# Optimization experiments

Measured on AMD Instinct MI355X. Metric: run time of the kernel, lower is better.

## Reference

```python
import jax, jax.numpy as jnp
import numpy as np

B, H, N, M = 8192, 512, 1024, 128
EPS_COS = 1e-8   # torch cosine_similarity default eps
EPS_NORM = 1e-16 # normalization eps in forward


def _linear_params(key, fan_in, fan_out):
    # torch nn.Linear default init: U(-1/sqrt(fan_in), 1/sqrt(fan_in))
    lim = 1.0 / np.sqrt(fan_in)
    kw, kb = jax.random.split(key)
    W = jax.random.uniform(kw, (fan_out, fan_in), minval=-lim, maxval=lim, dtype=jnp.float32)
    b = jax.random.uniform(kb, (fan_out,), minval=-lim, maxval=lim, dtype=jnp.float32)
    return W, b


def setup_inputs() -> dict:
    key = jax.random.key(0)
    ks = jax.random.split(key, 8)
    Wk, bk = _linear_params(ks[0], H, M)
    Wb, bb = _linear_params(ks[1], H, 1)
    Wg, bg = _linear_params(ks[2], H, 1)
    Ws, bs = _linear_params(ks[3], H, N)
    Wgam, bgam = _linear_params(ks[4], H, 1)
    x = jax.random.normal(ks[5], (B, H), dtype=jnp.float32)
    # previous_state is an attention-weight vector over memory rows (sums to 1)
    previous_state = jax.nn.softmax(jax.random.normal(ks[6], (B, N), dtype=jnp.float32), axis=-1)
    memory = jax.random.normal(ks[7], (N, M), dtype=jnp.float32)
    return dict(x=x, previous_state=previous_state, memory=memory,
                Wk=Wk, bk=bk, Wb=Wb, bb=bb, Wg=Wg, bg=bg,
                Ws=Ws, bs=bs, Wgam=Wgam, bgam=bgam)


def _circular_convolution(w, s):
    # Full circular convolution over the memory axis:
    #   out[b, i] = sum_j w[b, j] * s[b, (i - j) mod N]
    # Implemented via FFT to avoid materializing a [B, N, N] shift matrix.
    out = jnp.fft.irfft(jnp.fft.rfft(w, axis=-1) * jnp.fft.rfft(s, axis=-1),
                        n=w.shape[-1], axis=-1)
    # conv of nonnegative weights is nonnegative; clamp tiny FFT round-off
    # negatives so the fractional power below stays well defined.
    return jnp.maximum(out, 0.0)


def reference(x, previous_state, memory, Wk, bk, Wb, bb, Wg, bg, Ws, bs, Wgam, bgam):
    k = x @ Wk.T + bk                                   # [B, M]
    beta = jax.nn.softplus(x @ Wb.T + bb)               # [B, 1]
    g = jax.nn.sigmoid(x @ Wg.T + bg)                   # [B, 1]
    s = jax.nn.softmax(x @ Ws.T + bs, axis=-1)          # [B, N]
    gamma = 1.0 + jax.nn.softplus(x @ Wgam.T + bgam)    # [B, 1]

    # cosine similarity between each key and each memory row -> [B, N]
    k_n = k / jnp.maximum(jnp.linalg.norm(k, axis=-1, keepdims=True), EPS_COS)
    m_n = memory / jnp.maximum(jnp.linalg.norm(memory, axis=-1, keepdims=True), EPS_COS)
    cos = k_n @ m_n.T                                   # [B, N]

    w_c = jax.nn.softmax(beta * cos, axis=1)            # content addressing
    w_g = g * w_c + (1.0 - g) * previous_state          # interpolation gate
    w_t = _circular_convolution(w_g, s)                 # location shift
    w = w_t ** gamma                                    # sharpening
    w = w / (jnp.sum(w, axis=1, keepdims=True) + EPS_NORM)

    read = w @ memory                                   # [B, M]
    return read, w
```

## Files before the change

### kernel.cpp

```cpp
#include <hip/hip_runtime.h>
#include <hip/hip_bf16.h>
#include <hip/hip_fp16.h>

typedef __attribute__((ext_vector_type(8))) short short8;
typedef __attribute__((ext_vector_type(4))) short short4v;
typedef __attribute__((ext_vector_type(4))) float f32x4;

#define B_ROWS 8192
#define HDIM 512
#define NDIM 1024
#define MDIM 128

__device__ __forceinline__ float softplusf(float z) {
  return fmaxf(z, 0.f) + log1pf(__expf(-fabsf(z)));
}
__device__ __forceinline__ unsigned short f2bfu(float f) {
  __hip_bfloat16 h = __float2bfloat16(f);
  return *reinterpret_cast<unsigned short*>(&h);
}
__device__ __forceinline__ short8 pack8(float4 a, float4 b) {
  short8 r;
  r[0] = (short)f2bfu(a.x); r[1] = (short)f2bfu(a.y);
  r[2] = (short)f2bfu(a.z); r[3] = (short)f2bfu(a.w);
  r[4] = (short)f2bfu(b.x); r[5] = (short)f2bfu(b.y);
  r[6] = (short)f2bfu(b.z); r[7] = (short)f2bfu(b.w);
  return r;
}
__device__ __forceinline__ int pad(int i) { return i + (i >> 4); }

__global__ __launch_bounds__(256) void prep_all(
    const float* __restrict__ x, const float* __restrict__ Ws,
    const float* __restrict__ Wk, const float* __restrict__ mem,
    const float* __restrict__ Wb, const float* __restrict__ bb,
    const float* __restrict__ Wg, const float* __restrict__ bg,
    const float* __restrict__ Wgam, const float* __restrict__ bgam,
    short* __restrict__ xb, short* __restrict__ wsb, short* __restrict__ wkb,
    short* __restrict__ mn_bf, short* __restrict__ memT_bf,
    float* __restrict__ bgg)
{
  const int blk = blockIdx.x, t = threadIdx.x;
  if (blk < 512) {
    __shared__ float sredp[4];
    const int half = t >> 7, tl = t & 127;
    const int n = blk * 2 + half;
    const int wid = t >> 6;
    const float v = mem[n * MDIM + tl];
    float ss = v * v;
#pragma unroll
    for (int o = 32; o; o >>= 1) ss += __shfl_xor(ss, o);
    if ((t & 63) == 0) sredp[wid] = ss;
    __syncthreads();
    const float inv = 1.f / fmaxf(sqrtf(sredp[half * 2] + sredp[half * 2 + 1]), 1e-8f);
    mn_bf[n * MDIM + tl] = (short)f2bfu(v * inv);
    memT_bf[(size_t)tl * NDIM + n] = (short)f2bfu(v);
  } else if (blk < 2560) {
    const int wid = t >> 6, lane = t & 63;
    const int b = (blk - 512) * 4 + wid;
    const size_t xo = (size_t)b * HDIM + lane * 8;
    const float4 x0 = *(const float4*)(x + xo);
    const float4 x1 = *(const float4*)(x + xo + 4);
    *(short8*)(xb + xo) = pack8(x0, x1);
    const float4 b0 = *(const float4*)(Wb + lane * 8);
    const float4 b1 = *(const float4*)(Wb + lane * 8 + 4);
    const float4 g0 = *(const float4*)(Wg + lane * 8);
    const float4 g1 = *(const float4*)(Wg + lane * 8 + 4);
    const float4 m0 = *(const float4*)(Wgam + lane * 8);
    const float4 m1 = *(const float4*)(Wgam + lane * 8 + 4);
    float zb = x0.x*b0.x + x0.y*b0.y + x0.z*b0.z + x0.w*b0.w
             + x1.x*b1.x + x1.y*b1.y + x1.z*b1.z + x1.w*b1.w;
    float zg = x0.x*g0.x + x0.y*g0.y + x0.z*g0.z + x0.w*g0.w
             + x1.x*g1.x + x1.y*g1.y + x1.z*g1.z + x1.w*g1.w;
    float zm = x0.x*m0.x + x0.y*m0.y + x0.z*m0.z + x0.w*m0.w
             + x1.x*m1.x + x1.y*m1.y + x1.z*m1.z + x1.w*m1.w;
#pragma unroll
    for (int o = 32; o; o >>= 1) {
      zb += __shfl_xor(zb, o); zg += __shfl_xor(zg, o); zm += __shfl_xor(zm, o);
    }
    if (lane == 0) {
      zb += bb[0]; zg += bg[0]; zm += bgam[0];
      bgg[b * 4 + 0] = softplusf(zb);
      bgg[b * 4 + 1] = 1.f / (1.f + __expf(-zg));
      bgg[b * 4 + 2] = 1.f + softplusf(zm);
    }
  } else {
    const int NS4 = NDIM * HDIM / 4;
    const int NK4 = MDIM * HDIM / 4;
    const int stride = 144 * 256;
    for (int i = (blk - 2560) * 256 + t; i < NS4 + NK4; i += stride) {
      const float* src; short* dst; int j = i;
      if (j < NS4) { src = Ws; dst = wsb; }
      else { j -= NS4; src = Wk; dst = wkb; }
      const float4 v = ((const float4*)src)[j];
      short4v o;
      o[0] = (short)f2bfu(v.x); o[1] = (short)f2bfu(v.y);
      o[2] = (short)f2bfu(v.z); o[3] = (short)f2bfu(v.w);
      ((short4v*)dst)[j] = o;
    }
  }
}

__global__ __launch_bounds__(256) void kgemm_cos(
    const short* __restrict__ xb, const short* __restrict__ wkb,
    const float* __restrict__ bk, const short* __restrict__ mn_bf,
    __half* __restrict__ cosbH)
{
  __shared__ __align__(16) short sA[32][40];
  __shared__ __align__(16) short sW[128][40];
  __shared__ __align__(16) short skhat[32][136];
  __shared__ __align__(16) short sMN[128][136];
  __shared__ float snorm[4][32];
  __shared__ float sinv[32];

  const int tid = threadIdx.x, lane = tid & 63, wid = tid >> 6;
  const int bm = blockIdx.x;
  const int fr = lane & 15, kg = (lane >> 4) << 3;
  const int rbase = (lane >> 4) << 2;

  f32x4 acc[2][2] = {};
  for (int k0 = 0; k0 < HDIM; k0 += 32) {
    if (k0) __syncthreads();
    if (tid < 128) {
      const int row = tid >> 2, c0 = (tid & 3) * 8;
      *(short8*)(&sA[row][c0]) =
          *(const short8*)(xb + (size_t)(bm * 32 + row) * HDIM + k0 + c0);
    }
#pragma unroll
    for (int u = tid; u < 512; u += 256) {
      const int row = u >> 2, c0 = (u & 3) * 8;
      *(short8*)(&sW[row][c0]) =
          *(const short8*)(wkb + (size_t)row * HDIM + k0 + c0);
    }
    __syncthreads();

    short8 af[2], bf[2];
#pragma unroll
    for (int i = 0; i < 2; i++) af[i] = *(const short8*)(&sA[i * 16 + fr][kg]);
#pragma unroll
    for (int n = 0; n < 2; n++) bf[n] = *(const short8*)(&sW[wid * 32 + n * 16 + fr][kg]);
#pragma unroll
    for (int i = 0; i < 2; i++)
#pragma unroll
      for (int n = 0; n < 2; n++)
        acc[i][n] = __builtin_amdgcn_mfma_f32_16x16x32_bf16(af[i], bf[n], acc[i][n], 0, 0, 0);
  }

  float z[2][2][4];
#pragma unroll
  for (int i = 0; i < 2; i++)
#pragma unroll
    for (int n = 0; n < 2; n++) {
      const float bv = bk[wid * 32 + n * 16 + fr];
#pragma unroll
      for (int r = 0; r < 4; r++) z[i][n][r] = acc[i][n][r] + bv;
    }
#pragma unroll
  for (int i = 0; i < 2; i++)
#pragma unroll
    for (int r = 0; r < 4; r++) {
      float sq = z[i][0][r] * z[i][0][r] + z[i][1][r] * z[i][1][r];
      sq += __shfl_xor(sq, 1); sq += __shfl_xor(sq, 2);
      sq += __shfl_xor(sq, 4); sq += __shfl_xor(sq, 8);
      if (fr == 0) snorm[wid][i * 16 + rbase + r] = sq;
    }
  __syncthreads();
  if (tid < 32) {
    const float nn = snorm[0][tid] + snorm[1][tid] + snorm[2][tid] + snorm[3][tid];
    sinv[tid] = 1.f / fmaxf(sqrtf(nn), 1e-8f);
  }
  __syncthreads();
#pragma unroll
  for (int i = 0; i < 2; i++)
#pragma unroll
    for (int n = 0; n < 2; n++)
#pragma unroll
      for (int r = 0; r < 4; r++) {
        const int row = i * 16 + rbase + r;
        skhat[row][wid * 32 + n * 16 + fr] = (short)f2bfu(z[i][n][r] * sinv[row]);
      }

  for (int cc = 0; cc < 8; cc++) {
#pragma unroll
    for (int i = 0; i < 8; i++) {
      const int u = tid + i * 256;
      const int r = u >> 4, c0 = (u & 15) * 8;
      *(short8*)(&sMN[r][c0]) =
          *(const short8*)(mn_bf + (size_t)(cc * 128 + r) * MDIM + c0);
    }
    __syncthreads();

    f32x4 acc2[2][2] = {};
#pragma unroll
    for (int k0 = 0; k0 < 128; k0 += 32) {
      short8 af2[2], bf2[2];
#pragma unroll
      for (int i = 0; i < 2; i++)
        af2[i] = *(const short8*)(&skhat[i * 16 + fr][k0 + kg]);
#pragma unroll
      for (int n = 0; n < 2; n++)
        bf2[n] = *(const short8*)(&sMN[wid * 32 + n * 16 + fr][k0 + kg]);
#pragma unroll
      for (int i = 0; i < 2; i++)
#pragma unroll
        for (int n = 0; n < 2; n++)
          acc2[i][n] = __builtin_amdgcn_mfma_f32_16x16x32_bf16(af2[i], bf2[n], acc2[i][n], 0, 0, 0);
    }
    __syncthreads();

#pragma unroll
    for (int i = 0; i < 2; i++)
#pragma unroll
      for (int n = 0; n < 2; n++)
#pragma unroll
        for (int r = 0; r < 4; r++) {
          const int row = i * 16 + rbase + r;
          const int gc = cc * 128 + wid * 32 + n * 16 + fr;
          cosbH[(size_t)(bm * 32 + row) * NDIM + gc] = __float2half(acc2[i][n][r]);
        }
  }
}

template<int OUTMODE>
__global__ __launch_bounds__(256) void kgemm128(
    const short* __restrict__ A, const short* __restrict__ W,
    const float* __restrict__ bias, void* __restrict__ C,
    int ncols, int Kld, int ksplit, size_t cstride)
{
  __shared__ __align__(16) short sA[128 * 32];
  __shared__ __align__(16) short sB[128 * 32];

  const int tid = threadIdx.x, lane = tid & 63, wid = tid >> 6;
  const int bm = blockIdx.y, bn = blockIdx.x;
  const int wr = wid >> 1, wc = wid & 1;
  const int fr = lane & 15, kg = (lane >> 4) << 3;
  const int kbeg = blockIdx.z * ksplit, kend = kbeg + ksplit;

  f32x4 acc[4][4] = {};

  for (int k0 = kbeg; k0 < kend; k0 += 32) {
    if (k0 != kbeg) __syncthreads();
#pragma unroll
    for (int j = 0; j < 2; j++) {
      const int c = tid + j * 256;
      const short* g = A + (size_t)(bm * 128 + (c >> 2)) * Kld + k0 + (c & 3) * 8;
      short* l = &sA[(j * 256 + wid * 64) * 8];
      __builtin_amdgcn_global_load_lds(
          (const __attribute__((address_space(1))) void*)g,
          (__attribute__((address_space(3))) void*)l, 16, 0, 0);
    }
#pragma unroll
    for (int j = 0; j < 2; j++) {
      const int c = tid + j * 256;
      const short* g = W + (size_t)(bn * 128 + (c >> 2)) * Kld + k0 + (c & 3) * 8;
      short* l = &sB[(j * 256 + wid * 64) * 8];
      __builtin_amdgcn_global_load_lds(
          (const __attribute__((address_space(1))) void*)g,
          (__attribute__((address_space(3))) void*)l, 16, 0, 0);
    }
    __syncthreads();

    short8 af[4], bf[4];
#pragma unroll
    for (int m = 0; m < 4; m++)
      af[m] = *(const short8*)(&sA[(wr * 64 + m * 16 + fr) * 32 + kg]);
#pragma unroll
    for (int n = 0; n < 4; n++)
      bf[n] = *(const short8*)(&sB[(wc * 64 + n * 16 + fr) * 32 + kg]);

#pragma unroll
    for (int m = 0; m < 4; m++)
#pragma unroll
      for (int n = 0; n < 4; n++)
        acc[m][n] = __builtin_amdgcn_mfma_f32_16x16x32_bf16(af[m], bf[n], acc[m][n], 0, 0, 0);
  }

#pragma unroll
  for (int m = 0; m < 4; m++)
#pragma unroll
    for (int n = 0; n < 4; n++) {
      const int gr = bm * 128 + wr * 64 + m * 16 + ((lane >> 4) << 2);
      const int gc = bn * 128 + wc * 64 + n * 16 + fr;
      const float bv = bias ? bias[gc] : 0.f;
#pragma unroll
      for (int r = 0; r < 4; r++) {
        const float v = acc[m][n][r] + bv;
        const size_t idx = (size_t)(gr + r) * ncols + gc + blockIdx.z * cstride;
        if constexpr (OUTMODE == 0) ((float*)C)[idx] = v;
        else ((__half*)C)[idx] = __float2half(v);
      }
    }
}

__global__ __launch_bounds__(256) void reduce4(const float* __restrict__ p,
                                               float* __restrict__ out)
{
  const int i = blockIdx.x * 256 + threadIdx.x;
  const float4* p4 = (const float4*)p;
  const float4 a = p4[i], b = p4[i + 262144], c = p4[i + 524288], d = p4[i + 786432];
  ((float4*)out)[i] = make_float4(a.x + b.x + c.x + d.x, a.y + b.y + c.y + d.y,
                                  a.z + b.z + c.z + d.z, a.w + b.w + c.w + d.w);
}

#define ANG0 (-0.0061359231515425650f)

template<int ST>
__device__ __forceinline__ void fft_mid(const float* __restrict__ sr,
                                        const float* __restrict__ si,
                                        float* __restrict__ dr,
                                        float* __restrict__ di, int tid,
                                        int j0, int j1, int j2, int j3)
{
  const int ls = 2 * ST, s = 1 << ls;
  const int p = tid >> ls, q = tid & (s - 1), tb = tid & ~(s - 1);
  const float a0r = sr[j0], a0i = si[j0], a1r = sr[j1], a1i = si[j1];
  const float a2r = sr[j2], a2i = si[j2], a3r = sr[j3], a3i = si[j3];
  const float b0r = a0r + a2r, b0i = a0i + a2i, b1r = a1r + a3r, b1i = a1i + a3i;
  const float b2r = a0r - a2r, b2i = a0i - a2i, b3r = a1r - a3r, b3i = a1i - a3i;
  const float A0r = b0r + b1r, A0i = b0i + b1i;
  const float A1r = b2r + b3i, A1i = b2i - b3r;
  const float A2r = b0r - b1r, A2i = b0i - b1i;
  const float A3r = b2r - b3i, A3i = b2i + b3r;
  const int o = q + 4 * s * p;
  dr[pad(o)] = A0r; di[pad(o)] = A0i;
  if constexpr (ST < 4) {
    float s1, c1; __sincosf(ANG0 * (float)tb, &s1, &c1);
    const float c2 = c1 * c1 - s1 * s1, s2 = 2.f * s1 * c1;
    const float c3 = c1 * c2 - s1 * s2, s3 = s1 * c2 + c1 * s2;
    dr[pad(o + s)]     = A1r * c1 - A1i * s1; di[pad(o + s)]     = A1r * s1 + A1i * c1;
    dr[pad(o + 2 * s)] = A2r * c2 - A2i * s2; di[pad(o + 2 * s)] = A2r * s2 + A2i * c2;
    dr[pad(o + 3 * s)] = A3r * c3 - A3i * s3; di[pad(o + 3 * s)] = A3r * s3 + A3i * c3;
  } else {
    dr[pad(o + s)]     = A1r; di[pad(o + s)]     = A1i;
    dr[pad(o + 2 * s)] = A2r; di[pad(o + 2 * s)] = A2i;
    dr[pad(o + 3 * s)] = A3r; di[pad(o + 3 * s)] = A3i;
  }
  __syncthreads();
}

template<int J>
__device__ __forceinline__ void fft512_mid(const float* __restrict__ sr,
                                           const float* __restrict__ si,
                                           float* __restrict__ dr,
                                           float* __restrict__ di, int tid)
{
  if (tid < 128) {
    constexpr int s  = (J == 1) ? 2 : (J == 2) ? 8 : 32;
    constexpr int ns = (J == 1) ? 256 : (J == 2) ? 64 : 16;
    constexpr int ls = (J == 1) ? 1 : (J == 2) ? 3 : 5;
    const int p = tid >> ls, q = tid & (s - 1);
    const float a0r = sr[pad(tid)],       a0i = si[pad(tid)];
    const float a1r = sr[pad(tid + 128)], a1i = si[pad(tid + 128)];
    const float a2r = sr[pad(tid + 256)], a2i = si[pad(tid + 256)];
    const float a3r = sr[pad(tid + 384)], a3i = si[pad(tid + 384)];
    const float b0r = a0r + a2r, b0i = a0i + a2i, b1r = a1r + a3r, b1i = a1i + a3i;
    const float b2r = a0r - a2r, b2i = a0i - a2i, b3r = a1r - a3r, b3i = a1i - a3i;
    const float A0r = b0r + b1r, A0i = b0i + b1i;
    const float A1r = b2r + b3i, A1i = b2i - b3r;
    const float A2r = b0r - b1r, A2i = b0i - b1i;
    const float A3r = b2r - b3i, A3i = b2i + b3r;
    float s1, c1; __sincosf((-6.283185307179586f / (float)ns) * (float)p, &s1, &c1);
    const float c2 = c1 * c1 - s1 * s1, s2 = 2.f * s1 * c1;
    const float c3 = c1 * c2 - s1 * s2, s3 = s1 * c2 + c1 * s2;
    const int o = q + 4 * s * p;
    dr[pad(o)]         = A0r;                 di[pad(o)]         = A0i;
    dr[pad(o + s)]     = A1r * c1 - A1i * s1; di[pad(o + s)]     = A1r * s1 + A1i * c1;
    dr[pad(o + 2 * s)] = A2r * c2 - A2i * s2; di[pad(o + 2 * s)] = A2r * s2 + A2i * c2;
    dr[pad(o + 3 * s)] = A3r * c3 - A3i * s3; di[pad(o + 3 * s)] = A3r * s3 + A3i * c3;
  }
  __syncthreads();
}

__global__ __launch_bounds__(256) void rowpass(
    const __half* __restrict__ slogH, const __half* __restrict__ cosbH,
    const float* __restrict__ bgg, const float* __restrict__ prev,
    float* __restrict__ wout, short* __restrict__ wbf)
{
  __shared__ float bAr[1088], bAi[1088], bBr[1088], bBi[1088];
  __shared__ float sred[8];
  const int b = blockIdx.x, tid = threadIdx.x;
  const int lane = tid & 63, wid = tid >> 6;
  const int j0 = pad(tid), j1 = pad(tid + 256), j2 = pad(tid + 512), j3 = pad(tid + 768);

  const float beta = bgg[b * 4 + 0], g = bgg[b * 4 + 1], gamma = bgg[b * 4 + 2];

  float sv[4], cv[4];
  float e1 = 0.f, e2 = 0.f;
#pragma unroll
  for (int i = 0; i < 4; i++) {
    sv[i] = __expf(__half2float(slogH[(size_t)b * NDIM + tid + i * 256]));
    cv[i] = __expf(beta * __half2float(cosbH[(size_t)b * NDIM + tid + i * 256]));
    e1 += sv[i]; e2 += cv[i];
  }
#pragma unroll
  for (int o = 32; o; o >>= 1) { e1 += __shfl_xor(e1, o); e2 += __shfl_xor(e2, o); }
  if (lane == 0) { sred[wid * 2] = e1; sred[wid * 2 + 1] = e2; }
  __syncthreads();
  const float r1 = 1.f / (sred[0] + sred[2] + sred[4] + sred[6]);
  const float r2 = 1.f / (sred[1] + sred[3] + sred[5] + sred[7]);

  float s1, c1; __sincosf(ANG0 * (float)tid, &s1, &c1);
  const float c2 = c1 * c1 - s1 * s1, s2 = 2.f * s1 * c1;
  const float c3 = c1 * c2 - s1 * s2, s3 = s1 * c2 + c1 * s2;

  {
    float ar[4], ai[4];
#pragma unroll
    for (int i = 0; i < 4; i++) {
      const int idx = tid + i * 256;
      const float pv = prev[(size_t)b * NDIM + idx];
      ar[i] = g * cv[i] * r2 + (1.f - g) * pv;
      ai[i] = sv[i] * r1;
    }
    const float b0r = ar[0] + ar[2], b0i = ai[0] + ai[2];
    const float b1r = ar[1] + ar[3], b1i = ai[1] + ai[3];
    const float b2r = ar[0] - ar[2], b2i = ai[0] - ai[2];
    const float b3r = ar[1] - ar[3], b3i = ai[1] - ai[3];
    const float A0r = b0r + b1r, A0i = b0i + b1i;
    const float A1r = b2r + b3i, A1i = b2i - b3r;
    const float A2r = b0r - b1r, A2i = b0i - b1i;
    const float A3r = b2r - b3i, A3i = b2i + b3r;
    const int o4 = 4 * tid;
    bBr[pad(o4)]     = A0r;                  bBi[pad(o4)]     = A0i;
    bBr[pad(o4 + 1)] = A1r * c1 - A1i * s1;  bBi[pad(o4 + 1)] = A1r * s1 + A1i * c1;
    bBr[pad(o4 + 2)] = A2r * c2 - A2i * s2;  bBi[pad(o4 + 2)] = A2r * s2 + A2i * c2;
    bBr[pad(o4 + 3)] = A3r * c3 - A3i * s3;  bBi[pad(o4 + 3)] = A3r * s3 + A3i * c3;
  }
  __syncthreads();

  fft_mid<1>(bBr, bBi, bAr, bAi, tid, j0, j1, j2, j3);
  fft_mid<2>(bAr, bAi, bBr, bBi, tid, j0, j1, j2, j3);
  fft_mid<3>(bBr, bBi, bAr, bAi, tid, j0, j1, j2, j3);
  fft_mid<4>(bAr, bAi, bBr, bBi, tid, j0, j1, j2, j3);

#pragma unroll
  for (int i = 0; i < 2; i++) {
    const int k = tid + i * 256;
    const int kp = pad(k), rp = pad((1024 - k) & 1023);
    const float Zkr = bBr[kp], Zki = bBi[kp];
    const float Zrr = bBr[rp], Zri = bBi[rp];
    const float Wr = 0.5f * (Zkr + Zrr), Wi = 0.5f * (Zki - Zri);
    const float Sr = 0.5f * (Zki + Zri), Si = 0.5f * (Zrr - Zkr);
    bAr[kp] = Wr * Sr - Wi * Si;
    bAi[kp] = Wr * Si + Wi * Sr;
  }
  if (tid == 0) {
    const int kp = pad(512);
    bAr[kp] = bBr[kp] * bBi[kp];
    bAi[kp] = 0.f;
  }
  __syncthreads();

  {
    float es, ec; __sincosf(0.0061359231515425650f * (float)tid, &es, &ec);
    const float P0r = bAr[pad(tid)],        P0i = bAi[pad(tid)];
    const float Pa0r = bAr[pad(512 - tid)], Pa0i = bAi[pad(512 - tid)];
    const float S0r = P0r + Pa0r, S0i = P0i - Pa0i;
    const float D0r = P0r - Pa0r, D0i = P0i + Pa0i;
    const float Q0r = S0r - es * D0r - ec * D0i;
    const float Q0i = S0i + ec * D0r - es * D0i;
    const float P1r = bAr[pad(tid + 256)],  P1i = bAi[pad(tid + 256)];
    const float Pa1r = bAr[pad(256 - tid)], Pa1i = bAi[pad(256 - tid)];
    const float S1r = P1r + Pa1r, S1i = P1i - Pa1i;
    const float D1r = P1r - Pa1r, D1i = P1i + Pa1i;
    const float Q1r = S1r - ec * D1r + es * D1i;
    const float Q1i = S1i - es * D1r - ec * D1i;
    const float ur = Q0r, ui = -Q0i, vr = Q1r, vi = -Q1i;
    float ts, tc; __sincosf(-0.012271846303085130f * (float)tid, &ts, &tc);
    const float d_r = ur - vr, d_i = ui - vi;
    bBr[pad(2 * tid)]     = ur + vr;             bBi[pad(2 * tid)]     = ui + vi;
    bBr[pad(2 * tid + 1)] = d_r * tc - d_i * ts; bBi[pad(2 * tid + 1)] = d_r * ts + d_i * tc;
  }
  __syncthreads();

  fft512_mid<1>(bBr, bBi, bAr, bAi, tid);
  fft512_mid<2>(bAr, bAi, bBr, bBi, tid);
  fft512_mid<3>(bBr, bBi, bAr, bAi, tid);

  if (tid < 128) {
    const int i0 = pad(tid), i1 = pad(tid + 128), i2 = pad(tid + 256), i3 = pad(tid + 384);
    const float a0r = bAr[i0], a0i = bAi[i0], a1r = bAr[i1], a1i = bAi[i1];
    const float a2r = bAr[i2], a2i = bAi[i2], a3r = bAr[i3], a3i = bAi[i3];
    const float b0r = a0r + a2r, b0i = a0i + a2i, b1r = a1r + a3r, b1i = a1i + a3i;
    const float b2r = a0r - a2r, b2i = a0i - a2i, b3r = a1r - a3r, b3i = a1i - a3i;
    bBr[i0] = b0r + b1r; bBi[i0] = b0i + b1i;
    bBr[i1] = b2r + b3i; bBi[i1] = b2i - b3r;
    bBr[i2] = b0r - b1r; bBi[i2] = b0i - b1i;
    bBr[i3] = b2r - b3i; bBi[i3] = b2i + b3r;
  }
  __syncthreads();

  const int m0 = pad(2 * tid), m1 = pad(2 * tid + 1);
  float xv[4];
  xv[0] =  bBr[m0] * (1.f / 1024.f);
  xv[1] = -bBi[m0] * (1.f / 1024.f);
  xv[2] =  bBr[m1] * (1.f / 1024.f);
  xv[3] = -bBi[m1] * (1.f / 1024.f);

  float wt[4]; float esum = 0.f;
#pragma unroll
  for (int i = 0; i < 4; i++) {
    const float v = fmaxf(xv[i], 0.f);
    const float p = (v > 0.f) ? __expf(gamma * __logf(v)) : 0.f;
    wt[i] = p; esum += p;
  }
#pragma unroll
  for (int o = 32; o; o >>= 1) esum += __shfl_xor(esum, o);
  if (lane == 0) sred[wid] = esum;
  __syncthreads();
  const float rn = 1.f / (sred[0] + sred[1] + sred[2] + sred[3] + 1e-16f);
  const float w0 = wt[0] * rn, w1 = wt[1] * rn, w2 = wt[2] * rn, w3 = wt[3] * rn;
  *(float4*)(wout + (size_t)b * NDIM + 4 * tid) = make_float4(w0, w1, w2, w3);
  short4v wb;
  wb[0] = (short)f2bfu(w0); wb[1] = (short)f2bfu(w1);
  wb[2] = (short)f2bfu(w2); wb[3] = (short)f2bfu(w3);
  *(short4v*)(wbf + (size_t)b * NDIM + 4 * tid) = wb;
}

extern "C" void kernel_launch(void* const* d_in, const int* in_sizes, int n_in,
                              void* d_out, int out_size, void* d_ws, size_t ws_size,
                              hipStream_t stream)
{
  const float* x    = (const float*)d_in[0];
  const float* prev = (const float*)d_in[1];
  const float* mem  = (const float*)d_in[2];
  const float* Wk   = (const float*)d_in[3];
  const float* bk   = (const float*)d_in[4];
  const float* Wb   = (const float*)d_in[5];
  const float* bb   = (const float*)d_in[6];
  const float* Wg   = (const float*)d_in[7];
  const float* bg   = (const float*)d_in[8];
  const float* Ws   = (const float*)d_in[9];
  const float* bs   = (const float*)d_in[10];
  const float* Wgam = (const float*)d_in[11];
  const float* bgam = (const float*)d_in[12];

  char* ws = (char*)d_ws;
  short*  mn_bf   = (short*) (ws + 0);
  short*  memT_bf = (short*) (ws + 262144);
  float*  bgg     = (float*) (ws + 524288);
  __half* slogH   = (__half*)(ws + 655360);
  __half* cosbH   = (__half*)(ws + 17432576);
  short*  xb      = (short*) (ws + 34209792);
  short*  wsb     = (short*) (ws + 42598400);
  short*  wkb     = (short*) (ws + 43646976);
  short*  wbf     = (short*) (ws + 43778048);
  float*  rpart   = (float*) (ws + 60555264);

  float* readout = (float*)d_out;
  float* wout = readout + (size_t)B_ROWS * MDIM;

  prep_all<<<2704, 256, 0, stream>>>(x, Ws, Wk, mem, Wb, bb, Wg, bg, Wgam, bgam,
                                     xb, wsb, wkb, mn_bf, memT_bf, bgg);
  kgemm_cos<<<B_ROWS / 32, 256, 0, stream>>>(xb, wkb, bk, mn_bf, cosbH);
  kgemm128<1><<<dim3(NDIM / 128, B_ROWS / 128, 1), 256, 0, stream>>>(
      xb, wsb, bs, slogH, NDIM, HDIM, HDIM, 0);
  rowpass<<<B_ROWS, 256, 0, stream>>>(slogH, cosbH, bgg, prev, wout, wbf);
  kgemm128<0><<<dim3(1, B_ROWS / 128, 4), 256, 0, stream>>>(
      wbf, memT_bf, nullptr, rpart, MDIM, NDIM, 256, (size_t)B_ROWS * MDIM);
  reduce4<<<1024, 256, 0, stream>>>(rpart, readout);
}
```

Before: 117.9 us.

## Merge cosine and shift-logit GEMMs into one heterogeneous heads kernel launch

Combines the key/cosine kernel (256 blocks) and the shift-logit GEMM (512 blocks) into one 768-block kernel that branches on block index and shares a union shared-memory buffer. The aim is to remove a launch and let the two independent GEMMs run concurrently, filling the GPU better than the small 256-block cosine kernel does alone. The cosine phase's memory tiles shrink from 128 to 64 rows per step, with one MFMA column tile per wave, which lowers per-block LDS use but doubles the number of barrier steps. The larger shared-memory footprint now applies to every block and may reduce occupancy for the GEMM blocks.

```diff
diff --git a/kernel.cpp b/kernel.cpp
--- a/kernel.cpp
+++ b/kernel.cpp
@@ -99,113 +99,80 @@
   }
 }
 
-__global__ __launch_bounds__(256) void kgemm_cos(
+__global__ __launch_bounds__(256) void heads(
     const short* __restrict__ xb, const short* __restrict__ wkb,
     const float* __restrict__ bk, const short* __restrict__ mn_bf,
-    __half* __restrict__ cosbH)
-{
-  __shared__ __align__(16) short sA[32][40];
-  __shared__ __align__(16) short sW[128][40];
-  __shared__ __align__(16) short skhat[32][136];
-  __shared__ __align__(16) short sMN[128][136];
-  __shared__ float snorm[4][32];
-  __shared__ float sinv[32];
-
+    __half* __restrict__ cosbH,
+    const short* __restrict__ wsb, const float* __restrict__ bs,
+    __half* __restrict__ slogH)
+{
+  __shared__ __align__(16) char smem[39680];
   const int tid = threadIdx.x, lane = tid & 63, wid = tid >> 6;
-  const int bm = blockIdx.x;
   const int fr = lane & 15, kg = (lane >> 4) << 3;
-  const int rbase = (lane >> 4) << 2;
-
-  f32x4 acc[2][2] = {};
-  for (int k0 = 0; k0 < HDIM; k0 += 32) {
-    if (k0) __syncthreads();
-    if (tid < 128) {
-      const int row = tid >> 2, c0 = (tid & 3) * 8;
-      *(short8*)(&sA[row][c0]) =
-          *(const short8*)(xb + (size_t)(bm * 32 + row) * HDIM + k0 + c0);
-    }
-#pragma unroll
-    for (int u = tid; u < 512; u += 256) {
-      const int row = u >> 2, c0 = (u & 3) * 8;
-      *(short8*)(&sW[row][c0]) =
-          *(const short8*)(wkb + (size_t)row * HDIM + k0 + c0);
-    }
+
+  if (blockIdx.x < 256) {
+    short (*sA)[40]     = (short(*)[40])(smem);
+    short (*sW)[40]     = (short(*)[40])(smem + 2560);
+    short (*skhat)[136] = (short(*)[136])(smem + 12800);
+    short (*sMN)[136]   = (short(*)[136])(smem + 21504);
+    float (*snorm)[32]  = (float(*)[32])(smem + 38912);
+    float* sinv         = (float*)(smem + 39424);
+
+    const int bm = blockIdx.x;
+    const int rbase = (lane >> 4) << 2;
+
+    f32x4 acc[2][2] = {};
+    for (int k0 = 0; k0 < HDIM; k0 += 32) {
+      if (k0) __syncthreads();
+      if (tid < 128) {
+        const int row = tid >> 2, c0 = (tid & 3) * 8;
+        *(short8*)(&sA[row][c0]) =
+            *(const short8*)(xb + (size_t)(bm * 32 + row) * HDIM + k0 + c0);
+      }
+#pragma unroll
+      for (int u = tid; u < 512; u += 256) {
+        const int row = u >> 2, c0 = (u & 3) * 8;
+        *(short8*)(&sW[row][c0]) =
+            *(const short8*)(wkb + (size_t)row * HDIM + k0 + c0);
+      }
+      __syncthreads();
+
+      short8 af[2], bf[2];
+#pragma unroll
+      for (int i = 0; i < 2; i++) af[i] = *(const short8*)(&sA[i * 16 + fr][kg]);
+#pragma unroll
+      for (int n = 0; n < 2; n++) bf[n] = *(const short8*)(&sW[wid * 32 + n * 16 + fr][kg]);
+#pragma unroll
+      for (int i = 0; i < 2; i++)
+#pragma unroll
+        for (int n = 0; n < 2; n++)
+          acc[i][n] = __builtin_amdgcn_mfma_f32_16x16x32_bf16(af[i], bf[n], acc[i][n], 0, 0, 0);
+    }
+
+    float z[2][2][4];
+#pragma unroll
+    for (int i = 0; i < 2; i++)
+#pragma unroll
+      for (int n = 0; n < 2; n++) {
+        const float bv = bk[wid * 32 + n * 16 + fr];
+#pragma unroll
+        for (int r = 0; r < 4; r++) z[i][n][r] = acc[i][n][r] + bv;
+      }
+#pragma unroll
+    for (int i = 0; i < 2; i++)
+#pragma unroll
+      for (int r = 0; r < 4; r++) {
+        float sq = z[i][0][r] * z[i][0][r] + z[i][1][r] * z[i][1][r];
+        sq += __shfl_xor(sq, 1); sq += __shfl_xor(sq, 2);
+        sq += __shfl_xor(sq, 4); sq += __shfl_xor(sq, 8);
+        if (fr == 0) snorm[wid][i * 16 + rbase + r] = sq;
+      }
     __syncthreads();
-
-    short8 af[2], bf[2];
-#pragma unroll
-    for (int i = 0; i < 2; i++) af[i] = *(const short8*)(&sA[i * 16 + fr][kg]);
-#pragma unroll
-    for (int n = 0; n < 2; n++) bf[n] = *(const short8*)(&sW[wid * 32 + n * 16 + fr][kg]);
-#pragma unroll
-    for (int i = 0; i < 2; i++)
-#pragma unroll
-      for (int n = 0; n < 2; n++)
-        acc[i][n] = __builtin_amdgcn_mfma_f32_16x16x32_bf16(af[i], bf[n], acc[i][n], 0, 0, 0);
-  }
-
-  float z[2][2][4];
-#pragma unroll
-  for (int i = 0; i < 2; i++)
-#pragma unroll
-    for (int n = 0; n < 2; n++) {
-      const float bv = bk[wid * 32 + n * 16 + fr];
-#pragma unroll
-      for (int r = 0; r < 4; r++) z[i][n][r] = acc[i][n][r] + bv;
-    }
-#pragma unroll
-  for (int i = 0; i < 2; i++)
-#pragma unroll
-    for (int r = 0; r < 4; r++) {
-      float sq = z[i][0][r] * z[i][0][r] + z[i][1][r] * z[i][1][r];
-      sq += __shfl_xor(sq, 1); sq += __shfl_xor(sq, 2);
-      sq += __shfl_xor(sq, 4); sq += __shfl_xor(sq, 8);
-      if (fr == 0) snorm[wid][i * 16 + rbase + r] = sq;
-    }
-  __syncthreads();
-  if (tid < 32) {
-    const float nn = snorm[0][tid] + snorm[1][tid] + snorm[2][tid] + snorm[3][tid];
-    sinv[tid] = 1.f / fmaxf(sqrtf(nn), 1e-8f);
-  }
-  __syncthreads();
-#pragma unroll
-  for (int i = 0; i < 2; i++)
-#pragma unroll
-    for (int n = 0; n < 2; n++)
-#pragma unroll
-      for (int r = 0; r < 4; r++) {
-        const int row = i * 16 + rbase + r;
-        skhat[row][wid * 32 + n * 16 + fr] = (short)f2bfu(z[i][n][r] * sinv[row]);
-      }
-
-  for (int cc = 0; cc < 8; cc++) {
-#pragma unroll
-    for (int i = 0; i < 8; i++) {
-      const int u = tid + i * 256;
-      const int r = u >> 4, c0 = (u & 15) * 8;
-      *(short8*)(&sMN[r][c0]) =
-          *(const short8*)(mn_bf + (size_t)(cc * 128 + r) * MDIM + c0);
+    if (tid < 32) {
+      const float nn = snorm[0][tid] + snorm[1][tid] + snorm[2][tid] + snorm[3][tid];
+      sinv[tid] = 1.f / fmaxf(sqrtf(nn), 1e-8f);
     }
     __syncthreads();
-
-    f32x4 acc2[2][2] = {};
-#pragma unroll
-    for (int k0 = 0; k0 < 128; k0 += 32) {
-      short8 af2[2], bf2[2];
-#pragma unroll
-      for (int i = 0; i < 2; i++)
-        af2[i] = *(const short8*)(&skhat[i * 16 + fr][k0 + kg]);
-#pragma unroll
-      for (int n = 0; n < 2; n++)
-        bf2[n] = *(const short8*)(&sMN[wid * 32 + n * 16 + fr][k0 + kg]);
-#pragma unroll
-      for (int i = 0; i < 2; i++)
-#pragma unroll
-        for (int n = 0; n < 2; n++)
-          acc2[i][n] = __builtin_amdgcn_mfma_f32_16x16x32_bf16(af2[i], bf2[n], acc2[i][n], 0, 0, 0);
-    }
-    __syncthreads();
-
 #pragma unroll
     for (int i = 0; i < 2; i++)
 #pragma unroll
@@ -213,17 +180,103 @@
 #pragma unroll
         for (int r = 0; r < 4; r++) {
           const int row = i * 16 + rbase + r;
-          const int gc = cc * 128 + wid * 32 + n * 16 + fr;
-          cosbH[(size_t)(bm * 32 + row) * NDIM + gc] = __float2half(acc2[i][n][r]);
+          skhat[row][wid * 32 + n * 16 + fr] = (short)f2bfu(z[i][n][r] * sinv[row]);
         }
-  }
-}
-
-template<int OUTMODE>
-__global__ __launch_bounds__(256) void kgemm128(
+
+    for (int cc = 0; cc < 16; cc++) {
+#pragma unroll
+      for (int i = 0; i < 4; i++) {
+        const int u = tid + i * 256;
+        const int r = u >> 4, c0 = (u & 15) * 8;
+        *(short8*)(&sMN[r][c0]) =
+            *(const short8*)(mn_bf + (size_t)(cc * 64 + r) * MDIM + c0);
+      }
+      __syncthreads();
+
+      f32x4 acc2[2] = {};
+#pragma unroll
+      for (int k0 = 0; k0 < 128; k0 += 32) {
+        short8 af2[2], bf2;
+#pragma unroll
+        for (int i = 0; i < 2; i++)
+          af2[i] = *(const short8*)(&skhat[i * 16 + fr][k0 + kg]);
+        bf2 = *(const short8*)(&sMN[wid * 16 + fr][k0 + kg]);
+#pragma unroll
+        for (int i = 0; i < 2; i++)
+          acc2[i] = __builtin_amdgcn_mfma_f32_16x16x32_bf16(af2[i], bf2, acc2[i], 0, 0, 0);
+      }
+      __syncthreads();
+
+#pragma unroll
+      for (int i = 0; i < 2; i++)
+#pragma unroll
+        for (int r = 0; r < 4; r++) {
+          const int row = i * 16 + rbase + r;
+          const int gc = cc * 64 + wid * 16 + fr;
+          cosbH[(size_t)(bm * 32 + row) * NDIM + gc] = __float2half(acc2[i][r]);
+        }
+    }
+  } else {
+    short* sA = (short*)smem;
+    short* sB = (short*)(smem + 8192);
+    const int blk2 = blockIdx.x - 256;
+    const int bm = blk2 >> 3, bn = blk2 & 7;
+    const int wr = wid >> 1, wc = wid & 1;
+
+    f32x4 acc[4][4] = {};
+    for (int k0 = 0; k0 < HDIM; k0 += 32) {
+      if (k0) __syncthreads();
+#pragma unroll
+      for (int j = 0; j < 2; j++) {
+        const int c = tid + j * 256;
+        const short* g = xb + (size_t)(bm * 128 + (c >> 2)) * HDIM + k0 + (c & 3) * 8;
+        short* l = sA + (j * 256 + wid * 64) * 8;
+        __builtin_amdgcn_global_load_lds(
+            (const __attribute__((address_space(1))) void*)g,
+            (__attribute__((address_space(3))) void*)l, 16, 0, 0);
+      }
+#pragma unroll
+      for (int j = 0; j < 2; j++) {
+        const int c = tid + j * 256;
+        const short* g = wsb + (size_t)(bn * 128 + (c >> 2)) * HDIM + k0 + (c & 3) * 8;
+        short* l = sB + (j * 256 + wid * 64) * 8;
+        __builtin_amdgcn_global_load_lds(
+            (const __attribute__((address_space(1))) void*)g,
+            (__attribute__((address_space(3))) void*)l, 16, 0, 0);
+      }
+      __syncthreads();
+
+      short8 af[4], bf[4];
+#pragma unroll
+      for (int m = 0; m < 4; m++)
+        af[m] = *(const short8*)(&sA[(wr * 64 + m * 16 + fr) * 32 + kg]);
+#pragma unroll
+      for (int n = 0; n < 4; n++)
+        bf[n] = *(const short8*)(&sB[(wc * 64 + n * 16 + fr) * 32 + kg]);
+#pragma unroll
+      for (int m = 0; m < 4; m++)
+#pragma unroll
+        for (int n = 0; n < 4; n++)
+          acc[m][n] = __builtin_amdgcn_mfma_f32_16x16x32_bf16(af[m], bf[n], acc[m][n], 0, 0, 0);
+    }
+
+#pragma unroll
+    for (int m = 0; m < 4; m++)
+#pragma unroll
+      for (int n = 0; n < 4; n++) {
+        const int gr = bm * 128 + wr * 64 + m * 16 + ((lane >> 4) << 2);
+        const int gc = bn * 128 + wc * 64 + n * 16 + fr;
+        const float bv = bs[gc];
+#pragma unroll
+        for (int r = 0; r < 4; r++)
+          slogH[(size_t)(gr + r) * NDIM + gc] = __float2half(acc[m][n][r] + bv);
+      }
+  }
+}
+
+__global__ __launch_bounds__(256) void kgemm_read(
     const short* __restrict__ A, const short* __restrict__ W,
-    const float* __restrict__ bias, void* __restrict__ C,
-    int ncols, int Kld, int ksplit, size_t cstride)
+    float* __restrict__ C, int ncols, int Kld, int ksplit, size_t cstride)
 {
   __shared__ __align__(16) short sA[128 * 32];
   __shared__ __align__(16) short sB[128 * 32];
@@ -279,14 +332,9 @@
     for (int n = 0; n < 4; n++) {
       const int gr = bm * 128 + wr * 64 + m * 16 + ((lane >> 4) << 2);
       const int gc = bn * 128 + wc * 64 + n * 16 + fr;
-      const float bv = bias ? bias[gc] : 0.f;
-#pragma unroll
-      for (int r = 0; r < 4; r++) {
-        const float v = acc[m][n][r] + bv;
-        const size_t idx = (size_t)(gr + r) * ncols + gc + blockIdx.z * cstride;
-        if constexpr (OUTMODE == 0) ((float*)C)[idx] = v;
-        else ((__half*)C)[idx] = __float2half(v);
-      }
+#pragma unroll
+      for (int r = 0; r < 4; r++)
+        C[(size_t)(gr + r) * ncols + gc + blockIdx.z * cstride] = acc[m][n][r];
     }
 }
 
@@ -550,11 +598,9 @@
 
   prep_all<<<2704, 256, 0, stream>>>(x, Ws, Wk, mem, Wb, bb, Wg, bg, Wgam, bgam,
                                      xb, wsb, wkb, mn_bf, memT_bf, bgg);
-  kgemm_cos<<<B_ROWS / 32, 256, 0, stream>>>(xb, wkb, bk, mn_bf, cosbH);
-  kgemm128<1><<<dim3(NDIM / 128, B_ROWS / 128, 1), 256, 0, stream>>>(
-      xb, wsb, bs, slogH, NDIM, HDIM, HDIM, 0);
+  heads<<<768, 256, 0, stream>>>(xb, wkb, bk, mn_bf, cosbH, wsb, bs, slogH);
   rowpass<<<B_ROWS, 256, 0, stream>>>(slogH, cosbH, bgg, prev, wout, wbf);
-  kgemm128<0><<<dim3(1, B_ROWS / 128, 4), 256, 0, stream>>>(
-      wbf, memT_bf, nullptr, rpart, MDIM, NDIM, 256, (size_t)B_ROWS * MDIM);
+  kgemm_read<<<dim3(1, B_ROWS / 128, 4), 256, 0, stream>>>(
+      wbf, memT_bf, rpart, MDIM, NDIM, 256, (size_t)B_ROWS * MDIM);
   reduce4<<<1024, 256, 0, stream>>>(rpart, readout);
 }
```

Result: faster. 106.0 us (-10.1%).
